# Kernel optimization log

Measured on AMD Instinct MI355X. Metric: run time of the kernel, lower is better.

Reference implementation:

```python
import jax, jax.numpy as jnp
import numpy as np

N_NODES = 50000
N_EDGES = 800000
IN_CH = 64
OUT_CH = 32
HEADS = 4
OUT_DIM = OUT_CH * HEADS  # concat=True -> 128
NEG_SLOPE = 0.2


def setup_inputs() -> dict:
    key = jax.random.key(0)
    ks = jax.random.split(key, 10)
    x = jax.random.normal(ks[0], (N_NODES, IN_CH), dtype=jnp.float32)
    edge_index = jax.random.randint(ks[1], (2, N_EDGES), 0, N_NODES, dtype=jnp.int64)
    s = 1.0 / np.sqrt(IN_CH)
    lin_w = jax.random.uniform(ks[2], (OUT_DIM, IN_CH), jnp.float32, -s, s)
    att_src = jax.random.uniform(ks[3], (HEADS, OUT_CH), jnp.float32, -s, s)
    att_dst = jax.random.uniform(ks[4], (HEADS, OUT_CH), jnp.float32, -s, s)
    gat_bias = jnp.zeros((OUT_DIM,), jnp.float32)
    res_w = jax.random.uniform(ks[5], (OUT_DIM, IN_CH), jnp.float32, -s, s)
    res_b = jax.random.uniform(ks[6], (OUT_DIM,), jnp.float32, -s, s)
    ln_g = jnp.ones((OUT_DIM,), jnp.float32)
    ln_b = jnp.zeros((OUT_DIM,), jnp.float32)
    return {"x": x, "edge_index": edge_index, "lin_w": lin_w, "att_src": att_src,
            "att_dst": att_dst, "gat_bias": gat_bias, "res_w": res_w, "res_b": res_b,
            "ln_g": ln_g, "ln_b": ln_b}


def reference(x, edge_index, lin_w, att_src, att_dst, gat_bias, res_w, res_b, ln_g, ln_b):
    N = x.shape[0]
    H, C = att_src.shape
    # PyG GATConv default: add self-loops
    loops = jnp.arange(N, dtype=edge_index.dtype)
    src = jnp.concatenate([edge_index[0], loops])  # [E+N]
    dst = jnp.concatenate([edge_index[1], loops])
    # linear transform -> [N, H, C]
    xt = (x @ lin_w.T).reshape(N, H, C)
    # per-node attention halves [N, H]
    a_src = (xt * att_src[None]).sum(-1)
    a_dst = (xt * att_dst[None]).sum(-1)
    # per-edge raw score with LeakyReLU(0.2) -> [E+N, H]
    e = jax.nn.leaky_relu(a_src[src] + a_dst[dst], NEG_SLOPE)
    # edge-softmax grouped by destination node (numerically stable)
    emax = jax.ops.segment_max(e, dst, num_segments=N)
    emax = jnp.where(jnp.isfinite(emax), emax, 0.0)
    ex = jnp.exp(e - emax[dst])
    esum = jax.ops.segment_sum(ex, dst, num_segments=N)
    alpha = ex / (esum[dst] + 1e-16)  # [E+N, H]
    # weighted message passing + scatter-add; concat heads
    msg = xt[src] * alpha[:, :, None]  # [E+N, H, C]
    h = jax.ops.segment_sum(msg, dst, num_segments=N).reshape(N, H * C) + gat_bias
    # residual linear + LayerNorm + LeakyReLU(0.2)
    z = h + x @ res_w.T + res_b
    mu = z.mean(-1, keepdims=True)
    var = ((z - mu) ** 2).mean(-1, keepdims=True)
    zn = (z - mu) * jax.lax.rsqrt(var + 1e-5) * ln_g + ln_b
    return jax.nn.leaky_relu(zn, NEG_SLOPE)
```

## Files before the change

### kernel.cpp

```cpp
#include <hip/hip_runtime.h>
#include <hip/hip_bf16.h>
#include <hip/hip_fp16.h>

typedef __hip_bfloat16 bf16;
typedef __attribute__((ext_vector_type(8))) short bf16x8;
typedef __attribute__((ext_vector_type(4))) float f32x4;

#define IN_CH   64
#define OUT_DIM 128
#define HEADS   4
#define NEG     0.2f
#define WPITCH  72
#define OPITCH  136
#define CAP     64
#define FS      16
#define OVF_CAP 8192

__device__ __forceinline__ float lo_bf(unsigned int u) { return __uint_as_float(u << 16); }
__device__ __forceinline__ float hi_bf(unsigned int u) { return __uint_as_float(u & 0xffff0000u); }

__device__ __forceinline__ unsigned int pack_bf2(float a, float b) {
    unsigned int ua = (unsigned int)__bfloat16_as_ushort(__float2bfloat16(a));
    unsigned int ub = (unsigned int)__bfloat16_as_ushort(__float2bfloat16(b));
    return ua | (ub << 16);
}

__device__ __forceinline__ float ld(const void* p, size_t i, int isbf) {
    return isbf ? __bfloat162float(((const bf16*)p)[i]) : ((const float*)p)[i];
}

__device__ __forceinline__ int load_idx(const void* ei, int is64, long long pos) {
    if (is64) return (int)(((const long long*)ei)[pos]);
    return ((const int*)ei)[pos];
}

__device__ __forceinline__ int detect_is64(const int* ei) {
    int o = ei[1] | ei[3] | ei[5] | ei[7] | ei[9] | ei[11] | ei[13] | ei[15];
    return (o == 0) ? 1 : 0;
}
__device__ __forceinline__ int detect_isbf(const unsigned int* ln_g) {
    return (ln_g[0] == 0x3F803F80u) ? 1 : 0;
}

__global__ __launch_bounds__(256) void k0_zero(int* __restrict__ fill, long long n) {
    long long i = ((long long)blockIdx.x * 256 + threadIdx.x) * 4;
    if (i + 3 < n) {
        *(int4*)&fill[i] = make_int4(0, 0, 0, 0);
    } else {
        for (long long j = i; j < n; ++j) fill[j] = 0;
    }
}

__global__ __launch_bounds__(256, 3) void k1_transform(
    const void* __restrict__ x, const void* __restrict__ lin_w,
    const void* __restrict__ res_w, const void* __restrict__ att_src,
    const void* __restrict__ att_dst, const void* __restrict__ gat_bias,
    const void* __restrict__ res_b,
    const void* __restrict__ ei, int E,
    bf16* __restrict__ xt, bf16* __restrict__ resid,
    float* __restrict__ a_src, float* __restrict__ a_dst,
    int* __restrict__ fill, int* __restrict__ srcs_pad,
    unsigned long long* __restrict__ ovf, int* __restrict__ ovf_cnt,
    const void* __restrict__ ln_g, int N)
{
    __shared__ __align__(16) short wA[256 * WPITCH];
    __shared__ __align__(16) short xB[64 * WPITCH];
    int t = threadIdx.x;
    int is64 = detect_is64((const int*)ei);
    int isbf = detect_isbf((const unsigned int*)ln_g);

    const long long stride = (long long)gridDim.x * 256;
    long long i0 = (long long)blockIdx.x * 256 + t;
    int es[4], ed[4]; bool ev[4];
    #pragma unroll
    for (int q = 0; q < 4; q++) {
        long long j = i0 + (long long)q * stride;
        ev[q] = (j < E);
        es[q] = 0; ed[q] = 0;
        if (ev[q]) {
            es[q] = load_idx(ei, is64, j);
            ed[q] = load_idx(ei, is64, (long long)E + j);
        }
    }

    {
        const void* src = (t < 128) ? lin_w : res_w;
        int row = (t < 128) ? t : (t - 128);
        short* dst = &wA[t * WPITCH];
        if (isbf) {
            const uint4* p = (const uint4*)((const bf16*)src + (size_t)row * 64);
            #pragma unroll
            for (int q = 0; q < 8; q++) ((uint4*)dst)[q] = p[q];
        } else {
            const float4* p = (const float4*)((const float*)src + (size_t)row * 64);
            #pragma unroll
            for (int q = 0; q < 16; q++) {
                float4 f = p[q];
                ((unsigned int*)dst)[2 * q]     = pack_bf2(f.x, f.y);
                ((unsigned int*)dst)[2 * q + 1] = pack_bf2(f.z, f.w);
            }
        }
    }

    {
        int j = t >> 2, part = t & 3;
        int gj = blockIdx.x * 64 + j;
        short* dst = &xB[j * WPITCH + part * 16];
        if (gj < N) {
            if (isbf) {
                const uint4* p = (const uint4*)((const bf16*)x + (size_t)gj * 64 + part * 16);
                ((uint4*)dst)[0] = p[0];
                ((uint4*)dst)[1] = p[1];
            } else {
                const float4* p = (const float4*)((const float*)x + (size_t)gj * 64 + part * 16);
                #pragma unroll
                for (int q = 0; q < 4; q++) {
                    float4 f = p[q];
                    ((unsigned int*)dst)[2 * q]     = pack_bf2(f.x, f.y);
                    ((unsigned int*)dst)[2 * q + 1] = pack_bf2(f.z, f.w);
                }
            }
        } else {
            ((uint4*)dst)[0] = make_uint4(0, 0, 0, 0);
            ((uint4*)dst)[1] = make_uint4(0, 0, 0, 0);
        }
    }
    __syncthreads();

    int w = t >> 6, lane = t & 63;
    int c = lane & 15, q = lane >> 4;

    bf16x8 afr[4][2];
    #pragma unroll
    for (int mt = 0; mt < 4; mt++) {
        #pragma unroll
        for (int kh = 0; kh < 2; kh++)
            afr[mt][kh] = *(const bf16x8*)&wA[(w * 64 + mt * 16 + c) * WPITCH + kh * 32 + q * 8];
    }

    int slot[4];
    #pragma unroll
    for (int q2 = 0; q2 < 4; q2++) {
        slot[q2] = 0;
        if (ev[q2]) {
            if ((unsigned)es[q2] >= (unsigned)N) es[q2] = 0;
            if ((unsigned)ed[q2] >= (unsigned)N) ed[q2] = 0;
            slot[q2] = atomicAdd(&fill[(size_t)ed[q2] * FS], 1);
        }
    }
    for (long long j = i0 + 4 * stride; j < E; j += stride) {
        int s = load_idx(ei, is64, j);
        int d = load_idx(ei, is64, (long long)E + j);
        if ((unsigned)s >= (unsigned)N) s = 0;
        if ((unsigned)d >= (unsigned)N) d = 0;
        int sl = atomicAdd(&fill[(size_t)d * FS], 1);
        if (sl < CAP) {
            srcs_pad[(size_t)d * CAP + sl] = s;
        } else {
            int k = atomicAdd(ovf_cnt, 1);
            if (k < OVF_CAP)
                ovf[k] = ((unsigned long long)(unsigned)d << 32) | (unsigned)s;
        }
    }

    f32x4 acc[4][4];
    #pragma unroll
    for (int mt = 0; mt < 4; mt++)
        #pragma unroll
        for (int nt = 0; nt < 4; nt++)
            acc[mt][nt] = (f32x4){0.f, 0.f, 0.f, 0.f};

    #pragma unroll
    for (int nt = 0; nt < 4; nt++) {
        bf16x8 b0 = *(const bf16x8*)&xB[(nt * 16 + c) * WPITCH + q * 8];
        bf16x8 b1 = *(const bf16x8*)&xB[(nt * 16 + c) * WPITCH + 32 + q * 8];
        #pragma unroll
        for (int mt = 0; mt < 4; mt++) {
            acc[mt][nt] = __builtin_amdgcn_mfma_f32_16x16x32_bf16(afr[mt][0], b0, acc[mt][nt], 0, 0, 0);
            acc[mt][nt] = __builtin_amdgcn_mfma_f32_16x16x32_bf16(afr[mt][1], b1, acc[mt][nt], 0, 0, 0);
        }
    }

    int isres = (w >= 2);
    int chw = (w & 1) * 64;

    float rb[4][4], atS[4][4], atD[4][4];
    #pragma unroll
    for (int mt = 0; mt < 4; mt++) {
        int ch0 = chw + mt * 16 + q * 4;
        #pragma unroll
        for (int r = 0; r < 4; r++) {
            if (isres) {
                rb[mt][r] = ld(res_b, ch0 + r, isbf) + ld(gat_bias, ch0 + r, isbf);
            } else {
                atS[mt][r] = ld(att_src, ch0 + r, isbf);
                atD[mt][r] = ld(att_dst, ch0 + r, isbf);
            }
        }
    }

    #pragma unroll
    for (int nt = 0; nt < 4; nt++) {
        int gnode = blockIdx.x * 64 + nt * 16 + c;
        float pS0 = 0.f, pS1 = 0.f, pD0 = 0.f, pD1 = 0.f;
        #pragma unroll
        for (int mt = 0; mt < 4; mt++) {
            if (isres) {
                acc[mt][nt][0] += rb[mt][0];
                acc[mt][nt][1] += rb[mt][1];
                acc[mt][nt][2] += rb[mt][2];
                acc[mt][nt][3] += rb[mt][3];
            } else {
                float v0 = acc[mt][nt][0], v1 = acc[mt][nt][1];
                float v2 = acc[mt][nt][2], v3 = acc[mt][nt][3];
                float s = v0 * atS[mt][0] + v1 * atS[mt][1] + v2 * atS[mt][2] + v3 * atS[mt][3];
                float d = v0 * atD[mt][0] + v1 * atD[mt][1] + v2 * atD[mt][2] + v3 * atD[mt][3];
                if (mt < 2) { pS0 += s; pD0 += d; } else { pS1 += s; pD1 += d; }
            }
        }
        if (!isres) {
            pS0 += __shfl_xor(pS0, 16, 64); pS0 += __shfl_xor(pS0, 32, 64);
            pS1 += __shfl_xor(pS1, 16, 64); pS1 += __shfl_xor(pS1, 32, 64);
            pD0 += __shfl_xor(pD0, 16, 64); pD0 += __shfl_xor(pD0, 32, 64);
            pD1 += __shfl_xor(pD1, 16, 64); pD1 += __shfl_xor(pD1, 32, 64);
            if (q == 0 && gnode < N) {
                int hb = (w & 1) * 2;
                *(float2*)&a_src[(size_t)gnode * HEADS + hb] = make_float2(pS0, pS1);
                *(float2*)&a_dst[(size_t)gnode * HEADS + hb] = make_float2(pD0, pD1);
            }
        }
    }

    __syncthreads();
    unsigned int* sOut = (unsigned int*)wA;
    #pragma unroll
    for (int nt = 0; nt < 4; nt++) {
        int node = nt * 16 + c;
        #pragma unroll
        for (int mt = 0; mt < 4; mt++) {
            int chc = w * 64 + mt * 16 + q * 4;
            uint2 uu = make_uint2(pack_bf2(acc[mt][nt][0], acc[mt][nt][1]),
                                  pack_bf2(acc[mt][nt][2], acc[mt][nt][3]));
            *(uint2*)&sOut[node * OPITCH + (chc >> 1)] = uu;
        }
    }
    __syncthreads();

    int tile0 = blockIdx.x * 64;
    int nvalid = N - tile0; if (nvalid > 64) nvalid = 64;
    unsigned int* xtw = (unsigned int*)xt;
    unsigned int* rsw = (unsigned int*)resid;
    #pragma unroll
    for (int i = 0; i < 4; i++) {
        int uidx = i * 1024 + t * 4;
        int node = uidx >> 6;
        int c2   = uidx & 63;
        if (node < nvalid) {
            uint4 vx = *(uint4*)&sOut[node * OPITCH + c2];
            *(uint4*)&xtw[(size_t)(tile0 + node) * 64 + c2] = vx;
            uint4 vr = *(uint4*)&sOut[node * OPITCH + 64 + c2];
            *(uint4*)&rsw[(size_t)(tile0 + node) * 64 + c2] = vr;
        }
    }

    #pragma unroll
    for (int q2 = 0; q2 < 4; q2++) {
        if (ev[q2]) {
            if (slot[q2] < CAP) {
                srcs_pad[(size_t)ed[q2] * CAP + slot[q2]] = es[q2];
            } else {
                int k = atomicAdd(ovf_cnt, 1);
                if (k < OVF_CAP)
                    ovf[k] = ((unsigned long long)(unsigned)ed[q2] << 32) | (unsigned)es[q2];
            }
        }
    }
}

__global__ __launch_bounds__(256) void k3_gather(
    const int* __restrict__ fill, const int* __restrict__ srcs_pad,
    const unsigned long long* __restrict__ ovf, const int* __restrict__ ovf_cnt,
    const unsigned int* __restrict__ xtu, const unsigned int* __restrict__ residu,
    const float* __restrict__ a_src, const float* __restrict__ a_dst,
    const void* __restrict__ ln_g, const void* __restrict__ ln_b,
    void* __restrict__ out, int N)
{
    int node = (int)((blockIdx.x * 256 + threadIdx.x) >> 6);
    int lane = threadIdx.x & 63;
    if (node >= N) return;
    int isbf = detect_isbf((const unsigned int*)ln_g);
    int h = lane >> 4;

    int deg = fill[(size_t)node * FS];
    int end = deg < CAP ? deg : CAP;
    int myS = (lane < end) ? srcs_pad[(size_t)node * CAP + lane] : 0;

    float adh = a_dst[(size_t)node * HEADS + h];
    float ash = a_src[(size_t)node * HEADS + h];
    float e0 = ash + adh;
    e0 = e0 > 0.f ? e0 : e0 * NEG;
    float p = __expf(e0);
    unsigned int u = xtu[(size_t)node * 64 + lane];
    float acc0 = p * lo_bf(u);
    float acc1 = p * hi_bf(u);
    float esum = p;

    for (int ee = 0; ee < end; ee += 16) {
        int   sarr[16];
        float av[16];
        unsigned int uv[16];
        #pragma unroll
        for (int q = 0; q < 16; q++)
            sarr[q] = __shfl(myS, (ee + q) & 63, 64);
        #pragma unroll
        for (int q = 0; q < 16; q++)
            av[q] = a_src[(size_t)sarr[q] * HEADS + h];
        #pragma unroll
        for (int q = 0; q < 16; q++)
            uv[q] = xtu[(size_t)sarr[q] * 64 + lane];
        #pragma unroll
        for (int q = 0; q < 16; q++) {
            float sc = av[q] + adh;
            sc = sc > 0.f ? sc : sc * NEG;
            float pe = __expf(sc);
            pe = (ee + q < end) ? pe : 0.f;
            acc0 = fmaf(pe, lo_bf(uv[q]), acc0);
            acc1 = fmaf(pe, hi_bf(uv[q]), acc1);
            esum += pe;
        }
    }

    int oc = *ovf_cnt;
    if (oc > 0) {
        if (oc > OVF_CAP) oc = OVF_CAP;
        for (int k = 0; k < oc; k++) {
            unsigned long long pr = ovf[k];
            if ((int)(pr >> 32) == node) {
                int s = (int)(unsigned)pr;
                float as = a_src[(size_t)s * HEADS + h];
                float sc = as + adh;
                sc = sc > 0.f ? sc : sc * NEG;
                float pe = __expf(sc);
                unsigned int us = xtu[(size_t)s * 64 + lane];
                acc0 = fmaf(pe, lo_bf(us), acc0);
                acc1 = fmaf(pe, hi_bf(us), acc1);
                esum += pe;
            }
        }
    }

    float inv = 1.f / (esum + 1e-16f);
    unsigned int ur = residu[(size_t)node * 64 + lane];
    float z0 = fmaf(acc0, inv, lo_bf(ur));
    float z1 = fmaf(acc1, inv, hi_bf(ur));

    float s1 = z0 + z1;
    float s2 = z0 * z0 + z1 * z1;
    #pragma unroll
    for (int m = 1; m < 64; m <<= 1) {
        s1 += __shfl_xor(s1, m, 64);
        s2 += __shfl_xor(s2, m, 64);
    }
    float mu  = s1 * (1.0f / OUT_DIM);
    float var = s2 * (1.0f / OUT_DIM) - mu * mu;
    float rstd = rsqrtf(var + 1e-5f);
    int c0 = 2 * lane, c1 = 2 * lane + 1;
    float y0 = (z0 - mu) * rstd * ld(ln_g, c0, isbf) + ld(ln_b, c0, isbf);
    float y1 = (z1 - mu) * rstd * ld(ln_g, c1, isbf) + ld(ln_b, c1, isbf);
    y0 = y0 > 0.f ? y0 : y0 * NEG;
    y1 = y1 > 0.f ? y1 : y1 * NEG;
    if (isbf) {
        ((unsigned int*)out)[(size_t)node * 64 + lane] = pack_bf2(y0, y1);
    } else {
        ((float2*)out)[(size_t)node * 64 + lane] = make_float2(y0, y1);
    }
}

extern "C" void kernel_launch(void* const* d_in, const int* in_sizes, int n_in,
                              void* d_out, int out_size, void* d_ws, size_t ws_size,
                              hipStream_t stream)
{
    const void* x        = d_in[0];
    const void* ei       = d_in[1];
    const void* lin_w    = d_in[2];
    const void* att_src  = d_in[3];
    const void* att_dst  = d_in[4];
    const void* gat_bias = d_in[5];
    const void* res_w    = d_in[6];
    const void* res_b    = d_in[7];
    const void* ln_g     = d_in[8];
    const void* ln_b     = d_in[9];

    int N  = in_sizes[0] / IN_CH;
    int E  = in_sizes[1] / 2;

    int*   fill    = (int*)d_ws;
    int*   ovf_cnt = fill + (size_t)N * FS;
    float* a_src   = (float*)(ovf_cnt + 16);
    float* a_dst   = a_src + (size_t)N * HEADS;
    unsigned long long* ovf =
        (unsigned long long*)(((uintptr_t)(a_dst + (size_t)N * HEADS) + 7) & ~(uintptr_t)7);
    int*   srcs_pad = (int*)(ovf + OVF_CAP);
    bf16*  xt      = (bf16*)(srcs_pad + (size_t)N * CAP);
    bf16*  resid   = xt + (size_t)N * OUT_DIM;

    int tiles = (N + 63) / 64;
    long long nz = (long long)N * FS + 16;

    k0_zero<<<(int)((nz / 4 + 255) / 256), 256, 0, stream>>>(fill, nz);
    k1_transform<<<tiles, 256, 0, stream>>>(x, lin_w, res_w, att_src, att_dst,
                                            gat_bias, res_b, ei, E,
                                            xt, resid, a_src, a_dst,
                                            fill, srcs_pad, ovf, ovf_cnt,
                                            ln_g, N);
    k3_gather<<<(N + 3) / 4, 256, 0, stream>>>(fill, srcs_pad, ovf, ovf_cnt,
                                               (const unsigned int*)xt,
                                               (const unsigned int*)resid,
                                               a_src, a_dst, ln_g, ln_b,
                                               d_out, N);
}
```

Before: 194.7 us.

## Fuse zero, transform, and gather into one persistent cooperative kernel

```diff
diff --git a/kernel.cpp b/kernel.cpp
--- a/kernel.cpp
+++ b/kernel.cpp
@@ -1,6 +1,9 @@
 #include <hip/hip_runtime.h>
+#include <hip/hip_cooperative_groups.h>
 #include <hip/hip_bf16.h>
 #include <hip/hip_fp16.h>
+
+namespace cg = cooperative_groups;
 
 typedef __hip_bfloat16 bf16;
 typedef __attribute__((ext_vector_type(8))) short bf16x8;
@@ -42,39 +45,34 @@
     return (ln_g[0] == 0x3F803F80u) ? 1 : 0;
 }
 
-__global__ __launch_bounds__(256) void k0_zero(int* __restrict__ fill, long long n) {
-    long long i = ((long long)blockIdx.x * 256 + threadIdx.x) * 4;
-    if (i + 3 < n) {
-        *(int4*)&fill[i] = make_int4(0, 0, 0, 0);
-    } else {
-        for (long long j = i; j < n; ++j) fill[j] = 0;
-    }
-}
-
-__global__ __launch_bounds__(256, 3) void k1_transform(
+__global__ __launch_bounds__(256, 3) void k_fused(
     const void* __restrict__ x, const void* __restrict__ lin_w,
     const void* __restrict__ res_w, const void* __restrict__ att_src,
     const void* __restrict__ att_dst, const void* __restrict__ gat_bias,
-    const void* __restrict__ res_b,
+    const void* __restrict__ res_b, const void* __restrict__ ln_g,
+    const void* __restrict__ ln_b,
     const void* __restrict__ ei, int E,
     bf16* __restrict__ xt, bf16* __restrict__ resid,
     float* __restrict__ a_src, float* __restrict__ a_dst,
     int* __restrict__ fill, int* __restrict__ srcs_pad,
     unsigned long long* __restrict__ ovf, int* __restrict__ ovf_cnt,
-    const void* __restrict__ ln_g, int N)
+    void* __restrict__ out, int N, int tiles)
 {
+    cg::grid_group grid = cg::this_grid();
     __shared__ __align__(16) short wA[256 * WPITCH];
     __shared__ __align__(16) short xB[64 * WPITCH];
     int t = threadIdx.x;
+    int bid = blockIdx.x;
+    int nblk = gridDim.x;
     int is64 = detect_is64((const int*)ei);
     int isbf = detect_isbf((const unsigned int*)ln_g);
 
-    const long long stride = (long long)gridDim.x * 256;
-    long long i0 = (long long)blockIdx.x * 256 + t;
+    const long long estride = (long long)nblk * 256;
+    long long i0 = (long long)bid * 256 + t;
     int es[4], ed[4]; bool ev[4];
     #pragma unroll
     for (int q = 0; q < 4; q++) {
-        long long j = i0 + (long long)q * stride;
+        long long j = i0 + (long long)q * estride;
         ev[q] = (j < E);
         es[q] = 0; ed[q] = 0;
         if (ev[q]) {
@@ -84,59 +82,13 @@
     }
 
     {
-        const void* src = (t < 128) ? lin_w : res_w;
-        int row = (t < 128) ? t : (t - 128);
-        short* dst = &wA[t * WPITCH];
-        if (isbf) {
-            const uint4* p = (const uint4*)((const bf16*)src + (size_t)row * 64);
-            #pragma unroll
-            for (int q = 0; q < 8; q++) ((uint4*)dst)[q] = p[q];
-        } else {
-            const float4* p = (const float4*)((const float*)src + (size_t)row * 64);
-            #pragma unroll
-            for (int q = 0; q < 16; q++) {
-                float4 f = p[q];
-                ((unsigned int*)dst)[2 * q]     = pack_bf2(f.x, f.y);
-                ((unsigned int*)dst)[2 * q + 1] = pack_bf2(f.z, f.w);
-            }
-        }
-    }
-
-    {
-        int j = t >> 2, part = t & 3;
-        int gj = blockIdx.x * 64 + j;
-        short* dst = &xB[j * WPITCH + part * 16];
-        if (gj < N) {
-            if (isbf) {
-                const uint4* p = (const uint4*)((const bf16*)x + (size_t)gj * 64 + part * 16);
-                ((uint4*)dst)[0] = p[0];
-                ((uint4*)dst)[1] = p[1];
-            } else {
-                const float4* p = (const float4*)((const float*)x + (size_t)gj * 64 + part * 16);
-                #pragma unroll
-                for (int q = 0; q < 4; q++) {
-                    float4 f = p[q];
-                    ((unsigned int*)dst)[2 * q]     = pack_bf2(f.x, f.y);
-                    ((unsigned int*)dst)[2 * q + 1] = pack_bf2(f.z, f.w);
-                }
-            }
-        } else {
-            ((uint4*)dst)[0] = make_uint4(0, 0, 0, 0);
-            ((uint4*)dst)[1] = make_uint4(0, 0, 0, 0);
-        }
-    }
-    __syncthreads();
-
-    int w = t >> 6, lane = t & 63;
-    int c = lane & 15, q = lane >> 4;
-
-    bf16x8 afr[4][2];
-    #pragma unroll
-    for (int mt = 0; mt < 4; mt++) {
-        #pragma unroll
-        for (int kh = 0; kh < 2; kh++)
-            afr[mt][kh] = *(const bf16x8*)&wA[(w * 64 + mt * 16 + c) * WPITCH + kh * 32 + q * 8];
-    }
+        long long nz = (long long)N * FS + 16;
+        for (long long i = i0 * 4; i + 3 < nz; i += estride * 4)
+            *(int4*)&fill[i] = make_int4(0, 0, 0, 0);
+        long long rem = nz & ~3LL;
+        if (i0 == 0) for (long long j = rem; j < nz; ++j) fill[j] = 0;
+    }
+    grid.sync();
 
     int slot[4];
     #pragma unroll
@@ -148,7 +100,7 @@
             slot[q2] = atomicAdd(&fill[(size_t)ed[q2] * FS], 1);
         }
     }
-    for (long long j = i0 + 4 * stride; j < E; j += stride) {
+    for (long long j = i0 + 4 * estride; j < E; j += estride) {
         int s = load_idx(ei, is64, j);
         int d = load_idx(ei, is64, (long long)E + j);
         if ((unsigned)s >= (unsigned)N) s = 0;
@@ -163,104 +115,159 @@
         }
     }
 
-    f32x4 acc[4][4];
-    #pragma unroll
-    for (int mt = 0; mt < 4; mt++)
-        #pragma unroll
-        for (int nt = 0; nt < 4; nt++)
-            acc[mt][nt] = (f32x4){0.f, 0.f, 0.f, 0.f};
-
-    #pragma unroll
-    for (int nt = 0; nt < 4; nt++) {
-        bf16x8 b0 = *(const bf16x8*)&xB[(nt * 16 + c) * WPITCH + q * 8];
-        bf16x8 b1 = *(const bf16x8*)&xB[(nt * 16 + c) * WPITCH + 32 + q * 8];
+    int w = t >> 6, lane = t & 63;
+    int c = lane & 15, q = lane >> 4;
+
+    for (int tile = bid; tile < tiles; tile += nblk) {
+        {
+            const void* src = (t < 128) ? lin_w : res_w;
+            int row = (t < 128) ? t : (t - 128);
+            short* dst = &wA[t * WPITCH];
+            if (isbf) {
+                const uint4* p = (const uint4*)((const bf16*)src + (size_t)row * 64);
+                #pragma unroll
+                for (int qq = 0; qq < 8; qq++) ((uint4*)dst)[qq] = p[qq];
+            } else {
+                const float4* p = (const float4*)((const float*)src + (size_t)row * 64);
+                #pragma unroll
+                for (int qq = 0; qq < 16; qq++) {
+                    float4 f = p[qq];
+                    ((unsigned int*)dst)[2 * qq]     = pack_bf2(f.x, f.y);
+                    ((unsigned int*)dst)[2 * qq + 1] = pack_bf2(f.z, f.w);
+                }
+            }
+        }
+        {
+            int j = t >> 2, part = t & 3;
+            int gj = tile * 64 + j;
+            short* dst = &xB[j * WPITCH + part * 16];
+            if (gj < N) {
+                if (isbf) {
+                    const uint4* p = (const uint4*)((const bf16*)x + (size_t)gj * 64 + part * 16);
+                    ((uint4*)dst)[0] = p[0];
+                    ((uint4*)dst)[1] = p[1];
+                } else {
+                    const float4* p = (const float4*)((const float*)x + (size_t)gj * 64 + part * 16);
+                    #pragma unroll
+                    for (int qq = 0; qq < 4; qq++) {
+                        float4 f = p[qq];
+                        ((unsigned int*)dst)[2 * qq]     = pack_bf2(f.x, f.y);
+                        ((unsigned int*)dst)[2 * qq + 1] = pack_bf2(f.z, f.w);
+                    }
+                }
+            } else {
+                ((uint4*)dst)[0] = make_uint4(0, 0, 0, 0);
+                ((uint4*)dst)[1] = make_uint4(0, 0, 0, 0);
+            }
+        }
+        __syncthreads();
+
+        bf16x8 afr[4][2];
         #pragma unroll
         for (int mt = 0; mt < 4; mt++) {
-            acc[mt][nt] = __builtin_amdgcn_mfma_f32_16x16x32_bf16(afr[mt][0], b0, acc[mt][nt], 0, 0, 0);
-            acc[mt][nt] = __builtin_amdgcn_mfma_f32_16x16x32_bf16(afr[mt][1], b1, acc[mt][nt], 0, 0, 0);
-        }
-    }
-
-    int isres = (w >= 2);
-    int chw = (w & 1) * 64;
-
-    float rb[4][4], atS[4][4], atD[4][4];
-    #pragma unroll
-    for (int mt = 0; mt < 4; mt++) {
-        int ch0 = chw + mt * 16 + q * 4;
-        #pragma unroll
-        for (int r = 0; r < 4; r++) {
-            if (isres) {
-                rb[mt][r] = ld(res_b, ch0 + r, isbf) + ld(gat_bias, ch0 + r, isbf);
-            } else {
-                atS[mt][r] = ld(att_src, ch0 + r, isbf);
-                atD[mt][r] = ld(att_dst, ch0 + r, isbf);
-            }
-        }
-    }
-
-    #pragma unroll
-    for (int nt = 0; nt < 4; nt++) {
-        int gnode = blockIdx.x * 64 + nt * 16 + c;
-        float pS0 = 0.f, pS1 = 0.f, pD0 = 0.f, pD1 = 0.f;
+            #pragma unroll
+            for (int kh = 0; kh < 2; kh++)
+                afr[mt][kh] = *(const bf16x8*)&wA[(w * 64 + mt * 16 + c) * WPITCH + kh * 32 + q * 8];
+        }
+
+        f32x4 acc[4][4];
+        #pragma unroll
+        for (int mt = 0; mt < 4; mt++)
+            #pragma unroll
+            for (int nt = 0; nt < 4; nt++)
+                acc[mt][nt] = (f32x4){0.f, 0.f, 0.f, 0.f};
+
+        #pragma unroll
+        for (int nt = 0; nt < 4; nt++) {
+            bf16x8 b0 = *(const bf16x8*)&xB[(nt * 16 + c) * WPITCH + q * 8];
+            bf16x8 b1 = *(const bf16x8*)&xB[(nt * 16 + c) * WPITCH + 32 + q * 8];
+            #pragma unroll
+            for (int mt = 0; mt < 4; mt++) {
+                acc[mt][nt] = __builtin_amdgcn_mfma_f32_16x16x32_bf16(afr[mt][0], b0, acc[mt][nt], 0, 0, 0);
+                acc[mt][nt] = __builtin_amdgcn_mfma_f32_16x16x32_bf16(afr[mt][1], b1, acc[mt][nt], 0, 0, 0);
+            }
+        }
+
+        int isres = (w >= 2);
+        int chw = (w & 1) * 64;
+        float rb[4][4], atS[4][4], atD[4][4];
         #pragma unroll
         for (int mt = 0; mt < 4; mt++) {
-            if (isres) {
-                acc[mt][nt][0] += rb[mt][0];
-                acc[mt][nt][1] += rb[mt][1];
-                acc[mt][nt][2] += rb[mt][2];
-                acc[mt][nt][3] += rb[mt][3];
-            } else {
-                float v0 = acc[mt][nt][0], v1 = acc[mt][nt][1];
-                float v2 = acc[mt][nt][2], v3 = acc[mt][nt][3];
-                float s = v0 * atS[mt][0] + v1 * atS[mt][1] + v2 * atS[mt][2] + v3 * atS[mt][3];
-                float d = v0 * atD[mt][0] + v1 * atD[mt][1] + v2 * atD[mt][2] + v3 * atD[mt][3];
-                if (mt < 2) { pS0 += s; pD0 += d; } else { pS1 += s; pD1 += d; }
-            }
-        }
-        if (!isres) {
-            pS0 += __shfl_xor(pS0, 16, 64); pS0 += __shfl_xor(pS0, 32, 64);
-            pS1 += __shfl_xor(pS1, 16, 64); pS1 += __shfl_xor(pS1, 32, 64);
-            pD0 += __shfl_xor(pD0, 16, 64); pD0 += __shfl_xor(pD0, 32, 64);
-            pD1 += __shfl_xor(pD1, 16, 64); pD1 += __shfl_xor(pD1, 32, 64);
-            if (q == 0 && gnode < N) {
-                int hb = (w & 1) * 2;
-                *(float2*)&a_src[(size_t)gnode * HEADS + hb] = make_float2(pS0, pS1);
-                *(float2*)&a_dst[(size_t)gnode * HEADS + hb] = make_float2(pD0, pD1);
-            }
-        }
-    }
-
-    __syncthreads();
-    unsigned int* sOut = (unsigned int*)wA;
-    #pragma unroll
-    for (int nt = 0; nt < 4; nt++) {
-        int node = nt * 16 + c;
-        #pragma unroll
-        for (int mt = 0; mt < 4; mt++) {
-            int chc = w * 64 + mt * 16 + q * 4;
-            uint2 uu = make_uint2(pack_bf2(acc[mt][nt][0], acc[mt][nt][1]),
-                                  pack_bf2(acc[mt][nt][2], acc[mt][nt][3]));
-            *(uint2*)&sOut[node * OPITCH + (chc >> 1)] = uu;
-        }
-    }
-    __syncthreads();
-
-    int tile0 = blockIdx.x * 64;
-    int nvalid = N - tile0; if (nvalid > 64) nvalid = 64;
-    unsigned int* xtw = (unsigned int*)xt;
-    unsigned int* rsw = (unsigned int*)resid;
-    #pragma unroll
-    for (int i = 0; i < 4; i++) {
-        int uidx = i * 1024 + t * 4;
-        int node = uidx >> 6;
-        int c2   = uidx & 63;
-        if (node < nvalid) {
-            uint4 vx = *(uint4*)&sOut[node * OPITCH + c2];
-            *(uint4*)&xtw[(size_t)(tile0 + node) * 64 + c2] = vx;
-            uint4 vr = *(uint4*)&sOut[node * OPITCH + 64 + c2];
-            *(uint4*)&rsw[(size_t)(tile0 + node) * 64 + c2] = vr;
-        }
+            int ch0 = chw + mt * 16 + q * 4;
+            #pragma unroll
+            for (int r = 0; r < 4; r++) {
+                if (isres) {
+                    rb[mt][r] = ld(res_b, ch0 + r, isbf) + ld(gat_bias, ch0 + r, isbf);
+                } else {
+                    atS[mt][r] = ld(att_src, ch0 + r, isbf);
+                    atD[mt][r] = ld(att_dst, ch0 + r, isbf);
+                }
+            }
+        }
+        #pragma unroll
+        for (int nt = 0; nt < 4; nt++) {
+            int gnode = tile * 64 + nt * 16 + c;
+            float pS0 = 0.f, pS1 = 0.f, pD0 = 0.f, pD1 = 0.f;
+            #pragma unroll
+            for (int mt = 0; mt < 4; mt++) {
+                if (isres) {
+                    acc[mt][nt][0] += rb[mt][0];
+                    acc[mt][nt][1] += rb[mt][1];
+                    acc[mt][nt][2] += rb[mt][2];
+                    acc[mt][nt][3] += rb[mt][3];
+                } else {
+                    float v0 = acc[mt][nt][0], v1 = acc[mt][nt][1];
+                    float v2 = acc[mt][nt][2], v3 = acc[mt][nt][3];
+                    float s = v0 * atS[mt][0] + v1 * atS[mt][1] + v2 * atS[mt][2] + v3 * atS[mt][3];
+                    float d = v0 * atD[mt][0] + v1 * atD[mt][1] + v2 * atD[mt][2] + v3 * atD[mt][3];
+                    if (mt < 2) { pS0 += s; pD0 += d; } else { pS1 += s; pD1 += d; }
+                }
+            }
+            if (!isres) {
+                pS0 += __shfl_xor(pS0, 16, 64); pS0 += __shfl_xor(pS0, 32, 64);
+                pS1 += __shfl_xor(pS1, 16, 64); pS1 += __shfl_xor(pS1, 32, 64);
+                pD0 += __shfl_xor(pD0, 16, 64); pD0 += __shfl_xor(pD0, 32, 64);
+                pD1 += __shfl_xor(pD1, 16, 64); pD1 += __shfl_xor(pD1, 32, 64);
+                if (q == 0 && gnode < N) {
+                    int hb = (w & 1) * 2;
+                    *(float2*)&a_src[(size_t)gnode * HEADS + hb] = make_float2(pS0, pS1);
+                    *(float2*)&a_dst[(size_t)gnode * HEADS + hb] = make_float2(pD0, pD1);
+                }
+            }
+        }
+
+        __syncthreads();
+        unsigned int* sOut = (unsigned int*)wA;
+        #pragma unroll
+        for (int nt = 0; nt < 4; nt++) {
+            int node = nt * 16 + c;
+            #pragma unroll
+            for (int mt = 0; mt < 4; mt++) {
+                int chc = w * 64 + mt * 16 + q * 4;
+                uint2 uu = make_uint2(pack_bf2(acc[mt][nt][0], acc[mt][nt][1]),
+                                      pack_bf2(acc[mt][nt][2], acc[mt][nt][3]));
+                *(uint2*)&sOut[node * OPITCH + (chc >> 1)] = uu;
+            }
+        }
+        __syncthreads();
+
+        int tile0 = tile * 64;
+        int nvalid = N - tile0; if (nvalid > 64) nvalid = 64;
+        unsigned int* xtw = (unsigned int*)xt;
+        unsigned int* rsw = (unsigned int*)resid;
+        #pragma unroll
+        for (int i = 0; i < 4; i++) {
+            int uidx = i * 1024 + t * 4;
+            int node = uidx >> 6;
+            int c2   = uidx & 63;
+            if (node < nvalid) {
+                uint4 vx = *(uint4*)&sOut[node * OPITCH + c2];
+                *(uint4*)&xtw[(size_t)(tile0 + node) * 64 + c2] = vx;
+                uint4 vr = *(uint4*)&sOut[node * OPITCH + 64 + c2];
+                *(uint4*)&rsw[(size_t)(tile0 + node) * 64 + c2] = vr;
+            }
+        }
+        __syncthreads();
     }
 
     #pragma unroll
@@ -275,104 +282,106 @@
             }
         }
     }
-}
-
-__global__ __launch_bounds__(256) void k3_gather(
-    const int* __restrict__ fill, const int* __restrict__ srcs_pad,
-    const unsigned long long* __restrict__ ovf, const int* __restrict__ ovf_cnt,
-    const unsigned int* __restrict__ xtu, const unsigned int* __restrict__ residu,
-    const float* __restrict__ a_src, const float* __restrict__ a_dst,
-    const void* __restrict__ ln_g, const void* __restrict__ ln_b,
-    void* __restrict__ out, int N)
-{
-    int node = (int)((blockIdx.x * 256 + threadIdx.x) >> 6);
-    int lane = threadIdx.x & 63;
-    if (node >= N) return;
-    int isbf = detect_isbf((const unsigned int*)ln_g);
-    int h = lane >> 4;
-
-    int deg = fill[(size_t)node * FS];
-    int end = deg < CAP ? deg : CAP;
-    int myS = (lane < end) ? srcs_pad[(size_t)node * CAP + lane] : 0;
-
-    float adh = a_dst[(size_t)node * HEADS + h];
-    float ash = a_src[(size_t)node * HEADS + h];
-    float e0 = ash + adh;
-    e0 = e0 > 0.f ? e0 : e0 * NEG;
-    float p = __expf(e0);
-    unsigned int u = xtu[(size_t)node * 64 + lane];
-    float acc0 = p * lo_bf(u);
-    float acc1 = p * hi_bf(u);
-    float esum = p;
-
-    for (int ee = 0; ee < end; ee += 16) {
-        int   sarr[16];
-        float av[16];
-        unsigned int uv[16];
-        #pragma unroll
-        for (int q = 0; q < 16; q++)
-            sarr[q] = __shfl(myS, (ee + q) & 63, 64);
-        #pragma unroll
-        for (int q = 0; q < 16; q++)
-            av[q] = a_src[(size_t)sarr[q] * HEADS + h];
-        #pragma unroll
-        for (int q = 0; q < 16; q++)
-            uv[q] = xtu[(size_t)sarr[q] * 64 + lane];
-        #pragma unroll
-        for (int q = 0; q < 16; q++) {
-            float sc = av[q] + adh;
-            sc = sc > 0.f ? sc : sc * NEG;
-            float pe = __expf(sc);
-            pe = (ee + q < end) ? pe : 0.f;
-            acc0 = fmaf(pe, lo_bf(uv[q]), acc0);
-            acc1 = fmaf(pe, hi_bf(uv[q]), acc1);
-            esum += pe;
-        }
-    }
-
-    int oc = *ovf_cnt;
-    if (oc > 0) {
-        if (oc > OVF_CAP) oc = OVF_CAP;
-        for (int k = 0; k < oc; k++) {
-            unsigned long long pr = ovf[k];
-            if ((int)(pr >> 32) == node) {
-                int s = (int)(unsigned)pr;
-                float as = a_src[(size_t)s * HEADS + h];
-                float sc = as + adh;
+    grid.sync();
+
+    {
+        const unsigned int* xtu = (const unsigned int*)xt;
+        const unsigned int* residu = (const unsigned int*)resid;
+        int h = lane >> 4;
+        int hsel = lane & 48;
+        int esel = lane & 15;
+        int ngroups = (N + 3) >> 2;
+        for (int g = bid; g < ngroups; g += nblk) {
+            int node = g * 4 + w;
+            if (node >= N) continue;
+
+            int deg = fill[(size_t)node * FS];
+            int end = deg < CAP ? deg : CAP;
+            int myS = (lane < end) ? srcs_pad[(size_t)node * CAP + lane] : 0;
+
+            float adh = a_dst[(size_t)node * HEADS + h];
+            float ash = a_src[(size_t)node * HEADS + h];
+            float e0 = ash + adh;
+            e0 = e0 > 0.f ? e0 : e0 * NEG;
+            float p = __expf(e0);
+            unsigned int u = xtu[(size_t)node * 64 + lane];
+            float acc0 = p * lo_bf(u);
+            float acc1 = p * hi_bf(u);
+            float psum = 0.f;
+
+            for (int ee = 0; ee < end; ee += 16) {
+                int me = ee + esel;
+                int sme = __shfl(myS, me & 63, 64);
+                float a = a_src[(size_t)sme * HEADS + h];
+                unsigned int uv[16];
+                #pragma unroll
+                for (int qq = 0; qq < 16; qq++) {
+                    int sq = __shfl(myS, (ee + qq) & 63, 64);
+                    uv[qq] = xtu[(size_t)sq * 64 + lane];
+                }
+                float sc = a + adh;
                 sc = sc > 0.f ? sc : sc * NEG;
                 float pe = __expf(sc);
-                unsigned int us = xtu[(size_t)s * 64 + lane];
-                acc0 = fmaf(pe, lo_bf(us), acc0);
-                acc1 = fmaf(pe, hi_bf(us), acc1);
-                esum += pe;
-            }
-        }
-    }
-
-    float inv = 1.f / (esum + 1e-16f);
-    unsigned int ur = residu[(size_t)node * 64 + lane];
-    float z0 = fmaf(acc0, inv, lo_bf(ur));
-    float z1 = fmaf(acc1, inv, hi_bf(ur));
-
-    float s1 = z0 + z1;
-    float s2 = z0 * z0 + z1 * z1;
-    #pragma unroll
-    for (int m = 1; m < 64; m <<= 1) {
-        s1 += __shfl_xor(s1, m, 64);
-        s2 += __shfl_xor(s2, m, 64);
-    }
-    float mu  = s1 * (1.0f / OUT_DIM);
-    float var = s2 * (1.0f / OUT_DIM) - mu * mu;
-    float rstd = rsqrtf(var + 1e-5f);
-    int c0 = 2 * lane, c1 = 2 * lane + 1;
-    float y0 = (z0 - mu) * rstd * ld(ln_g, c0, isbf) + ld(ln_b, c0, isbf);
-    float y1 = (z1 - mu) * rstd * ld(ln_g, c1, isbf) + ld(ln_b, c1, isbf);
-    y0 = y0 > 0.f ? y0 : y0 * NEG;
-    y1 = y1 > 0.f ? y1 : y1 * NEG;
-    if (isbf) {
-        ((unsigned int*)out)[(size_t)node * 64 + lane] = pack_bf2(y0, y1);
-    } else {
-        ((float2*)out)[(size_t)node * 64 + lane] = make_float2(y0, y1);
+                pe = (me < end) ? pe : 0.f;
+                psum += pe;
+                #pragma unroll
+                for (int qq = 0; qq < 16; qq++) {
+                    float peq = __shfl(pe, hsel | qq, 64);
+                    acc0 = fmaf(peq, lo_bf(uv[qq]), acc0);
+                    acc1 = fmaf(peq, hi_bf(uv[qq]), acc1);
+                }
+            }
+            psum += __shfl_xor(psum, 1, 64);
+            psum += __shfl_xor(psum, 2, 64);
+            psum += __shfl_xor(psum, 4, 64);
+            psum += __shfl_xor(psum, 8, 64);
+            float esum = p + psum;
+
+            int oc = *ovf_cnt;
+            if (oc > 0) {
+                if (oc > OVF_CAP) oc = OVF_CAP;
+                for (int k = 0; k < oc; k++) {
+                    unsigned long long pr = ovf[k];
+                    if ((int)(pr >> 32) == node) {
+                        int s = (int)(unsigned)pr;
+                        float as = a_src[(size_t)s * HEADS + h];
+                        float sc = as + adh;
+                        sc = sc > 0.f ? sc : sc * NEG;
+                        float pe = __expf(sc);
+                        unsigned int us = xtu[(size_t)s * 64 + lane];
+                        acc0 = fmaf(pe, lo_bf(us), acc0);
+                        acc1 = fmaf(pe, hi_bf(us), acc1);
+                        esum += pe;
+                    }
+                }
+            }
+
+            float inv = 1.f / (esum + 1e-16f);
+            unsigned int ur = residu[(size_t)node * 64 + lane];
+            float z0 = fmaf(acc0, inv, lo_bf(ur));
+            float z1 = fmaf(acc1, inv, hi_bf(ur));
+
+            float s1 = z0 + z1;
+            float s2 = z0 * z0 + z1 * z1;
+            #pragma unroll
+            for (int m = 1; m < 64; m <<= 1) {
+                s1 += __shfl_xor(s1, m, 64);
+                s2 += __shfl_xor(s2, m, 64);
+            }
+            float mu  = s1 * (1.0f / OUT_DIM);
+            float var = s2 * (1.0f / OUT_DIM) - mu * mu;
+            float rstd = rsqrtf(var + 1e-5f);
+            int c0 = 2 * lane, c1 = 2 * lane + 1;
+            float y0 = (z0 - mu) * rstd * ld(ln_g, c0, isbf) + ld(ln_b, c0, isbf);
+            float y1 = (z1 - mu) * rstd * ld(ln_g, c1, isbf) + ld(ln_b, c1, isbf);
+            y0 = y0 > 0.f ? y0 : y0 * NEG;
+            y1 = y1 > 0.f ? y1 : y1 * NEG;
+            if (isbf) {
+                ((unsigned int*)out)[(size_t)node * 64 + lane] = pack_bf2(y0, y1);
+            } else {
+                ((float2*)out)[(size_t)node * 64 + lane] = make_float2(y0, y1);
+            }
+        }
     }
 }
 
@@ -405,17 +414,24 @@
     bf16*  resid   = xt + (size_t)N * OUT_DIM;
 
     int tiles = (N + 63) / 64;
-    long long nz = (long long)N * FS + 16;
-
-    k0_zero<<<(int)((nz / 4 + 255) / 256), 256, 0, stream>>>(fill, nz);
-    k1_transform<<<tiles, 256, 0, stream>>>(x, lin_w, res_w, att_src, att_dst,
-                                            gat_bias, res_b, ei, E,
-                                            xt, resid, a_src, a_dst,
-                                            fill, srcs_pad, ovf, ovf_cnt,
-                                            ln_g, N);
-    k3_gather<<<(N + 3) / 4, 256, 0, stream>>>(fill, srcs_pad, ovf, ovf_cnt,
-                                               (const unsigned int*)xt,
-                                               (const unsigned int*)resid,
-                                               a_src, a_dst, ln_g, ln_b,
-                                               d_out, N);
-}
+
+    static int g_grid = 0;
+    if (g_grid == 0) {
+        hipDeviceProp_t prop;
+        hipGetDeviceProperties(&prop, 0);
+        int nb = 0;
+        hipOccupancyMaxActiveBlocksPerMultiprocessor(&nb, k_fused, 256, 0);
+        if (nb < 1) nb = 1;
+        g_grid = prop.multiProcessorCount * nb;
+        if (g_grid < 64) g_grid = 64;
+    }
+
+    void* args[] = {
+        (void*)&x, (void*)&lin_w, (void*)&res_w, (void*)&att_src,
+        (void*)&att_dst, (void*)&gat_bias, (void*)&res_b, (void*)&ln_g,
+        (void*)&ln_b, (void*)&ei, (void*)&E, (void*)&xt, (void*)&resid,
+        (void*)&a_src, (void*)&a_dst, (void*)&fill, (void*)&srcs_pad,
+        (void*)&ovf, (void*)&ovf_cnt, (void*)&d_out, (void*)&N, (void*)&tiles
+    };
+    hipLaunchCooperativeKernel(k_fused, dim3(g_grid), dim3(256), args, 0, stream);
+}
```

Result: slower. 406.4 us (+108.7%).

## Split edge-bucket counters per XCD and share edge exps across lanes

Applied to the files above, without the earlier changes.

```diff
diff --git a/kernel.cpp b/kernel.cpp
--- a/kernel.cpp
+++ b/kernel.cpp
@@ -12,8 +12,9 @@
 #define NEG     0.2f
 #define WPITCH  72
 #define OPITCH  136
-#define CAP     64
-#define FS      16
+#define XCDS    8
+#define CAPX    16
+#define ROWI    (XCDS * CAPX)
 #define OVF_CAP 8192
 
 __device__ __forceinline__ float lo_bf(unsigned int u) { return __uint_as_float(u << 16); }
@@ -40,6 +41,12 @@
 }
 __device__ __forceinline__ int detect_isbf(const unsigned int* ln_g) {
     return (ln_g[0] == 0x3F803F80u) ? 1 : 0;
+}
+
+__device__ __forceinline__ unsigned xcd_id() {
+    unsigned x;
+    asm("s_getreg_b32 %0, hwreg(HW_REG_XCC_ID)" : "=s"(x));
+    return x & (XCDS - 1);
 }
 
 __global__ __launch_bounds__(256) void k0_zero(int* __restrict__ fill, long long n) {
@@ -68,6 +75,8 @@
     int t = threadIdx.x;
     int is64 = detect_is64((const int*)ei);
     int isbf = detect_isbf((const unsigned int*)ln_g);
+    unsigned xcd = xcd_id();
+    int* myfill = fill + (size_t)xcd * N;
 
     const long long stride = (long long)gridDim.x * 256;
     long long i0 = (long long)blockIdx.x * 256 + t;
@@ -145,7 +154,9 @@
         if (ev[q2]) {
             if ((unsigned)es[q2] >= (unsigned)N) es[q2] = 0;
             if ((unsigned)ed[q2] >= (unsigned)N) ed[q2] = 0;
-            slot[q2] = atomicAdd(&fill[(size_t)ed[q2] * FS], 1);
+            slot[q2] = __hip_atomic_fetch_add(&myfill[ed[q2]], 1,
+                                              __ATOMIC_RELAXED,
+                                              __HIP_MEMORY_SCOPE_WORKGROUP);
         }
     }
     for (long long j = i0 + 4 * stride; j < E; j += stride) {
@@ -153,9 +164,10 @@
         int d = load_idx(ei, is64, (long long)E + j);
         if ((unsigned)s >= (unsigned)N) s = 0;
         if ((unsigned)d >= (unsigned)N) d = 0;
-        int sl = atomicAdd(&fill[(size_t)d * FS], 1);
-        if (sl < CAP) {
-            srcs_pad[(size_t)d * CAP + sl] = s;
+        int sl = __hip_atomic_fetch_add(&myfill[d], 1, __ATOMIC_RELAXED,
+                                        __HIP_MEMORY_SCOPE_WORKGROUP);
+        if (sl < CAPX) {
+            srcs_pad[(size_t)d * ROWI + xcd * CAPX + sl] = s;
         } else {
             int k = atomicAdd(ovf_cnt, 1);
             if (k < OVF_CAP)
@@ -266,8 +278,8 @@
     #pragma unroll
     for (int q2 = 0; q2 < 4; q2++) {
         if (ev[q2]) {
-            if (slot[q2] < CAP) {
-                srcs_pad[(size_t)ed[q2] * CAP + slot[q2]] = es[q2];
+            if (slot[q2] < CAPX) {
+                srcs_pad[(size_t)ed[q2] * ROWI + xcd * CAPX + slot[q2]] = es[q2];
             } else {
                 int k = atomicAdd(ovf_cnt, 1);
                 if (k < OVF_CAP)
@@ -290,10 +302,29 @@
     if (node >= N) return;
     int isbf = detect_isbf((const unsigned int*)ln_g);
     int h = lane >> 4;
-
-    int deg = fill[(size_t)node * FS];
-    int end = deg < CAP ? deg : CAP;
-    int myS = (lane < end) ? srcs_pad[(size_t)node * CAP + lane] : 0;
+    int hsel = lane & 48;
+    int esel = lane & 15;
+
+    int P[XCDS + 1];
+    P[0] = 0;
+    #pragma unroll
+    for (int xx = 0; xx < XCDS; xx++) {
+        int cv = fill[(size_t)xx * N + node];
+        cv = cv < CAPX ? cv : CAPX;
+        P[xx + 1] = P[xx] + cv;
+    }
+    int deg = P[XCDS];
+    int end = deg < 64 ? deg : 64;
+
+    int xsel = 0, Ps = 0;
+    #pragma unroll
+    for (int xx = 1; xx < XCDS; xx++) {
+        bool ge = lane >= P[xx];
+        xsel = ge ? xx : xsel;
+        Ps   = ge ? P[xx] : Ps;
+    }
+    int slot = xsel * CAPX + (lane - Ps);
+    int myS = (lane < end) ? srcs_pad[(size_t)node * ROWI + slot] : 0;
 
     float adh = a_dst[(size_t)node * HEADS + h];
     float ash = a_src[(size_t)node * HEADS + h];
@@ -303,29 +334,53 @@
     unsigned int u = xtu[(size_t)node * 64 + lane];
     float acc0 = p * lo_bf(u);
     float acc1 = p * hi_bf(u);
-    float esum = p;
+    float psum = 0.f;
 
     for (int ee = 0; ee < end; ee += 16) {
-        int   sarr[16];
-        float av[16];
+        int me = ee + esel;
+        int sme = __shfl(myS, me & 63, 64);
+        float a = a_src[(size_t)sme * HEADS + h];
         unsigned int uv[16];
         #pragma unroll
-        for (int q = 0; q < 16; q++)
-            sarr[q] = __shfl(myS, (ee + q) & 63, 64);
-        #pragma unroll
-        for (int q = 0; q < 16; q++)
-            av[q] = a_src[(size_t)sarr[q] * HEADS + h];
-        #pragma unroll
-        for (int q = 0; q < 16; q++)
-            uv[q] = xtu[(size_t)sarr[q] * 64 + lane];
-        #pragma unroll
-        for (int q = 0; q < 16; q++) {
-            float sc = av[q] + adh;
+        for (int qq = 0; qq < 16; qq++) {
+            int sq = __shfl(myS, (ee + qq) & 63, 64);
+            uv[qq] = xtu[(size_t)sq * 64 + lane];
+        }
+        float sc = a + adh;
+        sc = sc > 0.f ? sc : sc * NEG;
+        float pe = __expf(sc);
+        pe = (me < end) ? pe : 0.f;
+        psum += pe;
+        #pragma unroll
+        for (int qq = 0; qq < 16; qq++) {
+            float peq = __shfl(pe, hsel | qq, 64);
+            acc0 = fmaf(peq, lo_bf(uv[qq]), acc0);
+            acc1 = fmaf(peq, hi_bf(uv[qq]), acc1);
+        }
+    }
+    psum += __shfl_xor(psum, 1, 64);
+    psum += __shfl_xor(psum, 2, 64);
+    psum += __shfl_xor(psum, 4, 64);
+    psum += __shfl_xor(psum, 8, 64);
+    float esum = p + psum;
+
+    if (deg > 64) {
+        for (int r2 = 64; r2 < deg; r2++) {
+            int x2 = 0, Ps2 = 0;
+            #pragma unroll
+            for (int xx = 1; xx < XCDS; xx++) {
+                bool ge = r2 >= P[xx];
+                x2  = ge ? xx : x2;
+                Ps2 = ge ? P[xx] : Ps2;
+            }
+            int s = srcs_pad[(size_t)node * ROWI + x2 * CAPX + (r2 - Ps2)];
+            float as = a_src[(size_t)s * HEADS + h];
+            float sc = as + adh;
             sc = sc > 0.f ? sc : sc * NEG;
             float pe = __expf(sc);
-            pe = (ee + q < end) ? pe : 0.f;
-            acc0 = fmaf(pe, lo_bf(uv[q]), acc0);
-            acc1 = fmaf(pe, hi_bf(uv[q]), acc1);
+            unsigned int us = xtu[(size_t)s * 64 + lane];
+            acc0 = fmaf(pe, lo_bf(us), acc0);
+            acc1 = fmaf(pe, hi_bf(us), acc1);
             esum += pe;
         }
     }
@@ -395,17 +450,17 @@
     int E  = in_sizes[1] / 2;
 
     int*   fill    = (int*)d_ws;
-    int*   ovf_cnt = fill + (size_t)N * FS;
+    int*   ovf_cnt = fill + (size_t)XCDS * N;
     float* a_src   = (float*)(ovf_cnt + 16);
     float* a_dst   = a_src + (size_t)N * HEADS;
     unsigned long long* ovf =
-        (unsigned long long*)(((uintptr_t)(a_dst + (size_t)N * HEADS) + 7) & ~(uintptr_t)7);
+        (unsigned long long*)(((uintptr_t)(a_dst + (size_t)N * HEADS) + 63) & ~(uintptr_t)63);
     int*   srcs_pad = (int*)(ovf + OVF_CAP);
-    bf16*  xt      = (bf16*)(srcs_pad + (size_t)N * CAP);
+    bf16*  xt      = (bf16*)(srcs_pad + (size_t)N * ROWI);
     bf16*  resid   = xt + (size_t)N * OUT_DIM;
 
     int tiles = (N + 63) / 64;
-    long long nz = (long long)N * FS + 16;
+    long long nz = (long long)XCDS * N + 16;
 
     k0_zero<<<(int)((nz / 4 + 255) / 256), 256, 0, stream>>>(fill, nz);
     k1_transform<<<tiles, 256, 0, stream>>>(x, lin_w, res_w, att_src, att_dst,
```

Measured after the change: 200.1 us. 2.8% more time.
